# Kernel tuning notes

Hardware: AMD Instinct MI355X
Metric: run time of the kernel (lower is better)

## Reference

```python
import jax, jax.numpy as jnp
import numpy as np

L, H, C, V, T_BLK = 12, 12, 768, 50257, 1024
D = C // H  # head dim = 64


def _layernorm(x, g, b, eps=1e-5):
    m = jnp.mean(x, axis=-1, keepdims=True)
    v = jnp.mean(jnp.square(x - m), axis=-1, keepdims=True)
    return (x - m) * jax.lax.rsqrt(v + eps) * g + b


def setup_inputs() -> dict:
    key = jax.random.key(0)
    ks = jax.random.split(key, 8)
    B, T = 8, 1024
    s = 0.02
    sp = 0.02 / np.sqrt(2 * L)  # c_proj special init
    return {
        "idx": jax.random.randint(ks[0], (B, T), 0, V, dtype=jnp.int32),
        "wte": jax.random.normal(ks[1], (V, C), jnp.float32) * s,
        "wpe": jax.random.normal(ks[2], (T_BLK, C), jnp.float32) * s,
        "ln1_g": jnp.ones((L, C), jnp.float32),
        "ln1_b": jnp.zeros((L, C), jnp.float32),
        "w_qkv": jax.random.normal(ks[3], (L, C, 3 * C), jnp.float32) * s,
        "b_qkv": jnp.zeros((L, 3 * C), jnp.float32),
        "w_ao": jax.random.normal(ks[4], (L, C, C), jnp.float32) * sp,
        "b_ao": jnp.zeros((L, C), jnp.float32),
        "ln2_g": jnp.ones((L, C), jnp.float32),
        "ln2_b": jnp.zeros((L, C), jnp.float32),
        "w_fc": jax.random.normal(ks[5], (L, C, 4 * C), jnp.float32) * s,
        "b_fc": jnp.zeros((L, 4 * C), jnp.float32),
        "w_mo": jax.random.normal(ks[6], (L, 4 * C, C), jnp.float32) * sp,
        "b_mo": jnp.zeros((L, C), jnp.float32),
        "lnf_g": jnp.ones((C,), jnp.float32),
        "lnf_b": jnp.zeros((C,), jnp.float32),
    }


def reference(idx, wte, wpe, ln1_g, ln1_b, w_qkv, b_qkv, w_ao, b_ao,
              ln2_g, ln2_b, w_fc, b_fc, w_mo, b_mo, lnf_g, lnf_b):
    B, T = idx.shape
    scale = 1.0 / np.sqrt(D)
    causal = jnp.tril(jnp.ones((T, T), dtype=bool))  # [T,T]

    x = wte[idx] + wpe[:T]  # [B,T,C]

    def block(x, p):
        g1, b1, wq, bq, wo, bo, g2, b2_, wf, bf, w2, b2m = p
        h = _layernorm(x, g1, b1)
        qkv = h @ wq + bq  # [B,T,3C]
        q, k, v = jnp.split(qkv, 3, axis=-1)
        q = q.reshape(B, T, H, D)
        k = k.reshape(B, T, H, D)
        v = v.reshape(B, T, H, D)
        att = jnp.einsum('bqhd,bkhd->bhqk', q, k) * scale
        att = jnp.where(causal, att, -jnp.inf)
        att = jax.nn.softmax(att, axis=-1)
        y = jnp.einsum('bhqk,bkhd->bqhd', att, v).reshape(B, T, C)
        x = x + y @ wo + bo
        h2 = _layernorm(x, g2, b2_)
        x = x + jax.nn.gelu(h2 @ wf + bf, approximate=False) @ w2 + b2m
        return x, None

    params = (ln1_g, ln1_b, w_qkv, b_qkv, w_ao, b_ao,
              ln2_g, ln2_b, w_fc, b_fc, w_mo, b_mo)
    x, _ = jax.lax.scan(block, x, params)

    x = _layernorm(x, lnf_g, lnf_b)
    # inference path: logits only for last position, lm_head tied to wte
    logits = x[:, -1:, :] @ wte.T  # [B,1,V]
    return logits
```

## Files before the change

### kernel.cpp

```cpp
#include <hip/hip_runtime.h>

#define B_ 8
#define T_ 1024
#define C_ 768
#define H_ 12
#define L_ 12
#define V_ 50257

typedef __bf16 bf16_t;
typedef __bf16 bf16x8 __attribute__((ext_vector_type(8)));
typedef __bf16 bf16x4 __attribute__((ext_vector_type(4)));
typedef float f32x4 __attribute__((ext_vector_type(4)));

__device__ __forceinline__ unsigned short f2bf(float f) {
  bf16_t h = (bf16_t)f;
  return __builtin_bit_cast(unsigned short, h);
}

__device__ __forceinline__ unsigned short bfbits(bf16_t h) {
  return __builtin_bit_cast(unsigned short, h);
}

template<int CTRL>
__device__ __forceinline__ float dppf(float x) {
  return __builtin_bit_cast(float, __builtin_amdgcn_update_dpp(
      0, __builtin_bit_cast(int, x), CTRL, 0xF, 0xF, true));
}
__device__ __forceinline__ float red16_max(float x) {
  x = fmaxf(x, dppf<0xB1>(x));
  x = fmaxf(x, dppf<0x4E>(x));
  x = fmaxf(x, dppf<0x124>(x));
  x = fmaxf(x, dppf<0x128>(x));
  return x;
}
__device__ __forceinline__ float red16_sum(float x) {
  x += dppf<0xB1>(x);
  x += dppf<0x4E>(x);
  x += dppf<0x124>(x);
  x += dppf<0x128>(x);
  return x;
}

__global__ __launch_bounds__(192) void embed_kernel(
    const int* __restrict__ idx, const float* __restrict__ wte,
    const float* __restrict__ wpe, float* __restrict__ xf)
{
  const int bt = blockIdx.x;
  const int t = bt & (T_ - 1);
  const int tok = idx[bt];
  const int c4 = threadIdx.x << 2;
  float4 a = *(const float4*)(wte + (size_t)tok * C_ + c4);
  float4 p = *(const float4*)(wpe + (size_t)t * C_ + c4);
  float4 r; r.x = a.x + p.x; r.y = a.y + p.y; r.z = a.z + p.z; r.w = a.w + p.w;
  *(float4*)(xf + (size_t)bt * C_ + c4) = r;
}

template<bool LAST>
__global__ __launch_bounds__(256) void ln_kernel(
    const float* __restrict__ x, const float* __restrict__ gw,
    const float* __restrict__ bw, unsigned short* __restrict__ obf,
    float* __restrict__ of)
{
  __shared__ float red[8];
  const size_t row = LAST ? ((size_t)blockIdx.x * T_ + (T_ - 1)) : (size_t)blockIdx.x;
  const float* xr = x + row * C_;
  const int t = threadIdx.x;
  float v0 = xr[t], v1 = xr[t + 256], v2 = xr[t + 512];
  float s = v0 + v1 + v2;
  #pragma unroll
  for (int off = 32; off; off >>= 1) s += __shfl_xor(s, off);
  if ((t & 63) == 0) red[t >> 6] = s;
  __syncthreads();
  const float mean = (red[0] + red[1] + red[2] + red[3]) * (1.0f / C_);
  const float d0 = v0 - mean, d1 = v1 - mean, d2 = v2 - mean;
  float ss = d0 * d0 + d1 * d1 + d2 * d2;
  #pragma unroll
  for (int off = 32; off; off >>= 1) ss += __shfl_xor(ss, off);
  if ((t & 63) == 0) red[4 + (t >> 6)] = ss;
  __syncthreads();
  const float var = (red[4] + red[5] + red[6] + red[7]) * (1.0f / C_);
  const float rs = rsqrtf(var + 1e-5f);
  float o0 = d0 * rs * gw[t] + bw[t];
  float o1 = d1 * rs * gw[t + 256] + bw[t + 256];
  float o2 = d2 * rs * gw[t + 512] + bw[t + 512];
  if (LAST) {
    float* orow = of + (size_t)blockIdx.x * C_;
    orow[t] = o0; orow[t + 256] = o1; orow[t + 512] = o2;
  } else {
    unsigned short* orow = obf + row * C_;
    orow[t] = f2bf(o0); orow[t + 256] = f2bf(o1); orow[t + 512] = f2bf(o2);
  }
}

__global__ __launch_bounds__(256) void cvtw4_kernel(
    const float* __restrict__ wq, const float* __restrict__ wa,
    const float* __restrict__ wf, const float* __restrict__ wm,
    unsigned short* __restrict__ out)
{
  __shared__ float tile[32][33];
  const int i = blockIdx.x;
  const float* W; unsigned short* Wt; int K, N, tix;
  if (i < 1728)      { W = wq; Wt = out;                 K = C_;     N = 3 * C_; tix = i; }
  else if (i < 2304) { W = wa; Wt = out + 3 * C_ * C_;   K = C_;     N = C_;     tix = i - 1728; }
  else if (i < 4608) { W = wf; Wt = out + 4 * C_ * C_;   K = C_;     N = 4 * C_; tix = i - 2304; }
  else               { W = wm; Wt = out + 8 * C_ * C_;   K = 4 * C_; N = C_;     tix = i - 4608; }
  const int ntx = N >> 5;
  const int kb = (tix / ntx) << 5, nb = (tix % ntx) << 5;
  const int t = threadIdx.x;
  {
    const int k = t >> 3, n4 = (t & 7) << 2;
    float4 v = *(const float4*)(W + (size_t)(kb + k) * N + nb + n4);
    tile[k][n4] = v.x; tile[k][n4 + 1] = v.y; tile[k][n4 + 2] = v.z; tile[k][n4 + 3] = v.w;
  }
  __syncthreads();
  {
    const int n = t >> 3, k4 = (t & 7) << 2;
    ushort4 o;
    o.x = f2bf(tile[k4][n]);     o.y = f2bf(tile[k4 + 1][n]);
    o.z = f2bf(tile[k4 + 2][n]); o.w = f2bf(tile[k4 + 3][n]);
    *(ushort4*)(Wt + (size_t)(nb + n) * K + kb + k4) = o;
  }
}

template<int EPI>
__global__ __launch_bounds__(256) void gemm_bt(
    const unsigned short* __restrict__ A, const unsigned short* __restrict__ Bt,
    const float* __restrict__ bias, float* __restrict__ Cf,
    unsigned short* __restrict__ Cb, int M, int N, int K)
{
  __shared__ unsigned short As[128 * 32];
  __shared__ unsigned short Bs[128 * 32];
  const int tid = threadIdx.x;
  const int lane = tid & 63;
  const int w = tid >> 6;
  const int wr = w >> 1, wc = w & 1;
  const int m0 = blockIdx.y * 128;
  const int n0 = blockIdx.x * 128;
  const int l15 = lane & 15, l4 = lane >> 4;

  f32x4 acc[4][4] = {};

  const int srow = lane >> 2;
  const int schunk = lane & 3;
  const size_t aBase = (size_t)(m0 + w * 16 + srow) * K + schunk * 8;
  const size_t bBase = (size_t)(n0 + w * 16 + srow) * K + schunk * 8;
  unsigned short* sA = As + (w * 16) * 32;
  unsigned short* sB = Bs + (w * 16) * 32;

  const int nk = K >> 5;
  for (int kt = 0; kt < nk; ++kt) {
    const int k0 = kt << 5;
    __syncthreads();
    __builtin_amdgcn_global_load_lds(
        (const __attribute__((address_space(1))) unsigned int*)(A + aBase + k0),
        (__attribute__((address_space(3))) unsigned int*)(sA), 16, 0, 0);
    __builtin_amdgcn_global_load_lds(
        (const __attribute__((address_space(1))) unsigned int*)(A + aBase + (size_t)64 * K + k0),
        (__attribute__((address_space(3))) unsigned int*)(sA + 64 * 32), 16, 0, 0);
    __builtin_amdgcn_global_load_lds(
        (const __attribute__((address_space(1))) unsigned int*)(Bt + bBase + k0),
        (__attribute__((address_space(3))) unsigned int*)(sB), 16, 0, 0);
    __builtin_amdgcn_global_load_lds(
        (const __attribute__((address_space(1))) unsigned int*)(Bt + bBase + (size_t)64 * K + k0),
        (__attribute__((address_space(3))) unsigned int*)(sB + 64 * 32), 16, 0, 0);
    __syncthreads();

    bf16x8 af[4], bfr[4];
    const unsigned short* aw = As + wr * 64 * 32;
    const unsigned short* bw = Bs + wc * 64 * 32;
    #pragma unroll
    for (int mf = 0; mf < 4; ++mf)
      af[mf] = *(const bf16x8*)(aw + (mf * 16 + l15) * 32 + l4 * 8);
    #pragma unroll
    for (int nf = 0; nf < 4; ++nf)
      bfr[nf] = *(const bf16x8*)(bw + (nf * 16 + l15) * 32 + l4 * 8);
    #pragma unroll
    for (int mf = 0; mf < 4; ++mf) {
      #pragma unroll
      for (int nf = 0; nf < 4; ++nf)
        acc[mf][nf] = __builtin_amdgcn_mfma_f32_16x16x32_bf16(af[mf], bfr[nf], acc[mf][nf], 0, 0, 0);
    }
  }

  #pragma unroll
  for (int mf = 0; mf < 4; ++mf) {
    #pragma unroll
    for (int nf = 0; nf < 4; ++nf) {
      const int col = n0 + wc * 64 + nf * 16 + l15;
      const float bv = bias[col];
      int hh = 0, dd = 0;
      unsigned short* qkvo = nullptr;
      if constexpr (EPI == 3) {
        const int which = col / C_;
        const int rem = col - which * C_;
        hh = rem >> 6; dd = rem & 63;
        qkvo = Cb + (size_t)which * ((size_t)B_ * H_ * T_ * 64);
      }
      #pragma unroll
      for (int i = 0; i < 4; ++i) {
        const int row = m0 + wr * 64 + mf * 16 + l4 * 4 + i;
        float v = acc[mf][nf][i] + bv;
        if constexpr (EPI == 0) {
          Cf[(size_t)row * N + col] = v;
        } else if constexpr (EPI == 1) {
          Cf[(size_t)row * N + col] += v;
        } else if constexpr (EPI == 2) {
          float g = 0.5f * v * (1.0f + erff(v * 0.70710678118f));
          Cb[(size_t)row * N + col] = f2bf(g);
        } else {
          const int bb = row >> 10, tt = row & (T_ - 1);
          qkvo[(((size_t)bb * H_ + hh) * T_ + tt) * 64 + dd] = f2bf(v);
        }
      }
    }
  }
}

__global__ __launch_bounds__(256) void attn_kernel(
    const unsigned short* __restrict__ Qb, const unsigned short* __restrict__ Kb,
    const unsigned short* __restrict__ Vb, unsigned short* __restrict__ y)
{
  const int pb = blockIdx.x / 96;
  const int bh = blockIdx.x % 96;
  const int h = bh % H_;
  const int b = bh / H_;
  const int tid = threadIdx.x, lane = tid & 63, w = tid >> 6;
  const int l15 = lane & 15, l4 = lane >> 4;

  const int qw = (w < 2) ? (pb * 64 + w * 32) : ((15 - pb) * 64 + (w - 2) * 32);
  const int NT = (17 - pb) >> 1;

  __shared__ unsigned short Ks[128 * 64];
  __shared__ unsigned short Vt[64 * 136];
  __shared__ unsigned short Pb[4][32 * 74];

  const unsigned short* qp = Qb + ((size_t)bh * T_ + qw) * 64;
  bf16x8 qf[2][2];
  #pragma unroll
  for (int mf = 0; mf < 2; ++mf)
    #pragma unroll
    for (int ks = 0; ks < 2; ++ks)
      qf[mf][ks] = *(const bf16x8*)(qp + (mf * 16 + l15) * 64 + ks * 32 + l4 * 8);

  f32x4 o[2][4] = {};
  float mrow[2][4], lrow[2][4];
  #pragma unroll
  for (int mf = 0; mf < 2; ++mf)
    #pragma unroll
    for (int i = 0; i < 4; ++i) { mrow[mf][i] = -1e30f; lrow[mf][i] = 0.0f; }

  const unsigned short* kb0 = Kb + (size_t)bh * T_ * 64;
  const unsigned short* vb0 = Vb + (size_t)bh * T_ * 64;
  const int ck = w;
  const int skey = lane;
  const int sw = (skey & 7);

  bf16x8 kr0, kr1, kr2, kr3, vr0, vr1, vr2, vr3;
  {
    const unsigned short* kp = kb0 + (size_t)skey * 64;
    const unsigned short* vp = vb0 + (size_t)skey * 64;
    kr0 = *(const bf16x8*)(kp + ck * 8);
    kr1 = *(const bf16x8*)(kp + (ck + 4) * 8);
    kr2 = *(const bf16x8*)(kp + 64 * 64 + ck * 8);
    kr3 = *(const bf16x8*)(kp + 64 * 64 + (ck + 4) * 8);
    vr0 = *(const bf16x8*)(vp + ck * 8);
    vr1 = *(const bf16x8*)(vp + (ck + 4) * 8);
    vr2 = *(const bf16x8*)(vp + 64 * 64 + ck * 8);
    vr3 = *(const bf16x8*)(vp + 64 * 64 + (ck + 4) * 8);
  }

  for (int kt = 0; kt < NT; ++kt) {
    const int k0 = kt << 7;
    __syncthreads();
    *(bf16x8*)(Ks + skey * 64 + ((ck ^ sw) * 8)) = kr0;
    *(bf16x8*)(Ks + skey * 64 + (((ck + 4) ^ sw) * 8)) = kr1;
    *(bf16x8*)(Ks + (skey + 64) * 64 + ((ck ^ sw) * 8)) = kr2;
    *(bf16x8*)(Ks + (skey + 64) * 64 + (((ck + 4) ^ sw) * 8)) = kr3;
    #pragma unroll
    for (int j = 0; j < 8; ++j) {
      Vt[(ck * 8 + j) * 136 + skey]            = bfbits(vr0[j]);
      Vt[((ck + 4) * 8 + j) * 136 + skey]      = bfbits(vr1[j]);
      Vt[(ck * 8 + j) * 136 + skey + 64]       = bfbits(vr2[j]);
      Vt[((ck + 4) * 8 + j) * 136 + skey + 64] = bfbits(vr3[j]);
    }
    __syncthreads();
    if (kt + 1 < NT) {
      const int kn = (kt + 1) << 7;
      const unsigned short* kp = kb0 + (size_t)(kn + skey) * 64;
      const unsigned short* vp = vb0 + (size_t)(kn + skey) * 64;
      kr0 = *(const bf16x8*)(kp + ck * 8);
      kr1 = *(const bf16x8*)(kp + (ck + 4) * 8);
      kr2 = *(const bf16x8*)(kp + 64 * 64 + ck * 8);
      kr3 = *(const bf16x8*)(kp + 64 * 64 + (ck + 4) * 8);
      vr0 = *(const bf16x8*)(vp + ck * 8);
      vr1 = *(const bf16x8*)(vp + (ck + 4) * 8);
      vr2 = *(const bf16x8*)(vp + 64 * 64 + ck * 8);
      vr3 = *(const bf16x8*)(vp + 64 * 64 + (ck + 4) * 8);
    }

    #pragma unroll
    for (int h2 = 0; h2 < 2; ++h2) {
      const int kh0 = k0 + h2 * 64;
      if (kh0 > qw + 31) continue;

      f32x4 s[2][4] = {};
      __builtin_amdgcn_s_setprio(1);
      #pragma unroll
      for (int ks = 0; ks < 2; ++ks) {
        #pragma unroll
        for (int nfk = 0; nfk < 4; ++nfk) {
          const int key = h2 * 64 + nfk * 16 + l15;
          bf16x8 kf = *(const bf16x8*)(Ks + key * 64 + ((((ks << 2) | l4) ^ (l15 & 7)) * 8));
          #pragma unroll
          for (int mf = 0; mf < 2; ++mf)
            s[mf][nfk] = __builtin_amdgcn_mfma_f32_16x16x32_bf16(qf[mf][ks], kf, s[mf][nfk], 0, 0, 0);
        }
      }
      __builtin_amdgcn_s_setprio(0);

      #pragma unroll
      for (int mf = 0; mf < 2; ++mf) {
        const int qrow = qw + mf * 16 + l4 * 4;
        const bool fullt = (kh0 + 63) <= (qw + mf * 16);
        float alpha[4];
        float pvv[4][4];
        #pragma unroll
        for (int i = 0; i < 4; ++i) {
          const int q = qrow + i;
          float sv[4], tm = -1e30f;
          #pragma unroll
          for (int nfk = 0; nfk < 4; ++nfk) {
            float x = s[mf][nfk][i] * 0.125f;
            sv[nfk] = fullt ? x : ((kh0 + nfk * 16 + l15 <= q) ? x : -1e30f);
            tm = fmaxf(tm, sv[nfk]);
          }
          tm = red16_max(tm);
          const float mnew = fmaxf(mrow[mf][i], tm);
          alpha[i] = __expf(mrow[mf][i] - mnew);
          mrow[mf][i] = mnew;
          float rsum = 0.0f;
          #pragma unroll
          for (int nfk = 0; nfk < 4; ++nfk) {
            const float p = __expf(sv[nfk] - mnew);
            pvv[nfk][i] = p; rsum += p;
          }
          rsum = red16_sum(rsum);
          lrow[mf][i] = lrow[mf][i] * alpha[i] + rsum;
        }
        #pragma unroll
        for (int nf = 0; nf < 4; ++nf)
          #pragma unroll
          for (int i = 0; i < 4; ++i)
            o[mf][nf][i] *= alpha[i];
        #pragma unroll
        for (int nfk = 0; nfk < 4; ++nfk)
          #pragma unroll
          for (int i = 0; i < 4; ++i)
            Pb[w][(mf * 16 + l4 * 4 + i) * 74 + nfk * 16 + l15] = f2bf(pvv[nfk][i]);
      }

      bf16x8 pa[2][2];
      #pragma unroll
      for (int mf = 0; mf < 2; ++mf)
        #pragma unroll
        for (int k2 = 0; k2 < 2; ++k2)
          pa[mf][k2] = *(const bf16x8*)(Pb[w] + (mf * 16 + l15) * 74 + k2 * 32 + l4 * 8);
      __builtin_amdgcn_s_setprio(1);
      #pragma unroll
      for (int nf = 0; nf < 4; ++nf) {
        const int d = nf * 16 + l15;
        #pragma unroll
        for (int k2 = 0; k2 < 2; ++k2) {
          bf16x8 vf = *(const bf16x8*)(Vt + d * 136 + h2 * 64 + k2 * 32 + l4 * 8);
          #pragma unroll
          for (int mf = 0; mf < 2; ++mf)
            o[mf][nf] = __builtin_amdgcn_mfma_f32_16x16x32_bf16(pa[mf][k2], vf, o[mf][nf], 0, 0, 0);
        }
      }
      __builtin_amdgcn_s_setprio(0);
    }
  }

  #pragma unroll
  for (int mf = 0; mf < 2; ++mf) {
    #pragma unroll
    for (int i = 0; i < 4; ++i) {
      const float inv = 1.0f / lrow[mf][i];
      const int q = qw + mf * 16 + l4 * 4 + i;
      unsigned short* yr = y + (size_t)(b * T_ + q) * C_ + h * 64;
      #pragma unroll
      for (int nf = 0; nf < 4; ++nf)
        yr[nf * 16 + l15] = f2bf(o[mf][nf][i] * inv);
    }
  }
}

__global__ __launch_bounds__(256) void head_kernel(
    const float* __restrict__ lnf, const float* __restrict__ wte,
    float* __restrict__ out)
{
  __shared__ float xs[B_ * C_];
  for (int i = threadIdx.x; i < B_ * C_; i += 256) xs[i] = lnf[i];
  __syncthreads();
  const int w = threadIdx.x >> 6, lane = threadIdx.x & 63;
  const int v = blockIdx.x * 4 + w;
  if (v >= V_) return;
  const float* wv = wte + (size_t)v * C_ + lane * 12;
  float4 w0 = *(const float4*)(wv);
  float4 w1 = *(const float4*)(wv + 4);
  float4 w2 = *(const float4*)(wv + 8);
  float acc[B_];
  #pragma unroll
  for (int bb = 0; bb < B_; ++bb) {
    const float* xr = xs + bb * C_ + lane * 12;
    float4 x0 = *(const float4*)(xr);
    float4 x1 = *(const float4*)(xr + 4);
    float4 x2 = *(const float4*)(xr + 8);
    acc[bb] = w0.x * x0.x + w0.y * x0.y + w0.z * x0.z + w0.w * x0.w
            + w1.x * x1.x + w1.y * x1.y + w1.z * x1.z + w1.w * x1.w
            + w2.x * x2.x + w2.y * x2.y + w2.z * x2.z + w2.w * x2.w;
  }
  #pragma unroll
  for (int off = 32; off; off >>= 1) {
    #pragma unroll
    for (int bb = 0; bb < B_; ++bb)
      acc[bb] += __shfl_xor(acc[bb], off);
  }
  if (lane == 0) {
    #pragma unroll
    for (int bb = 0; bb < B_; ++bb)
      out[(size_t)bb * V_ + v] = acc[bb];
  }
}

extern "C" void kernel_launch(void* const* d_in, const int* in_sizes, int n_in,
                              void* d_out, int out_size, void* d_ws, size_t ws_size,
                              hipStream_t stream)
{
  (void)in_sizes; (void)n_in; (void)out_size; (void)ws_size;
  const int*   idx   = (const int*)d_in[0];
  const float* wte   = (const float*)d_in[1];
  const float* wpe   = (const float*)d_in[2];
  const float* ln1_g = (const float*)d_in[3];
  const float* ln1_b = (const float*)d_in[4];
  const float* w_qkv = (const float*)d_in[5];
  const float* b_qkv = (const float*)d_in[6];
  const float* w_ao  = (const float*)d_in[7];
  const float* b_ao  = (const float*)d_in[8];
  const float* ln2_g = (const float*)d_in[9];
  const float* ln2_b = (const float*)d_in[10];
  const float* w_fc  = (const float*)d_in[11];
  const float* b_fc  = (const float*)d_in[12];
  const float* w_mo  = (const float*)d_in[13];
  const float* b_mo  = (const float*)d_in[14];
  const float* lnf_g = (const float*)d_in[15];
  const float* lnf_b = (const float*)d_in[16];

  char* ws = (char*)d_ws;
  size_t off = 0;
  auto wsalloc = [&](size_t bytes) -> void* {
    void* p = ws + off;
    off += (bytes + 255) & ~(size_t)255;
    return p;
  };
  const size_t SZH = (size_t)B_ * H_ * T_ * 64;
  float* xf             = (float*)wsalloc((size_t)B_ * T_ * C_ * 4);
  unsigned short* qkv3  = (unsigned short*)wsalloc(3 * SZH * 2);
  unsigned short* a_in  = (unsigned short*)wsalloc((size_t)B_ * T_ * C_ * 2);
  unsigned short* act2  = (unsigned short*)wsalloc((size_t)B_ * T_ * 4 * C_ * 2);
  unsigned short* wbuf  = (unsigned short*)wsalloc((size_t)12 * C_ * C_ * 2);
  float* lnfb           = (float*)wsalloc((size_t)B_ * C_ * 4);

  const size_t OFF_AO = (size_t)3 * C_ * C_;
  const size_t OFF_FC = (size_t)4 * C_ * C_;
  const size_t OFF_MO = (size_t)8 * C_ * C_;

  embed_kernel<<<B_ * T_, 192, 0, stream>>>(idx, wte, wpe, xf);

  for (int l = 0; l < L_; ++l) {
    ln_kernel<false><<<B_ * T_, 256, 0, stream>>>(xf, ln1_g + l * C_, ln1_b + l * C_, a_in, nullptr);
    cvtw4_kernel<<<6912, 256, 0, stream>>>(
        w_qkv + (size_t)l * C_ * 3 * C_, w_ao + (size_t)l * C_ * C_,
        w_fc + (size_t)l * C_ * 4 * C_, w_mo + (size_t)l * 4 * C_ * C_, wbuf);
    gemm_bt<3><<<dim3(3 * C_ / 128, B_ * T_ / 128), 256, 0, stream>>>(a_in, wbuf, b_qkv + l * 3 * C_, nullptr, qkv3, B_ * T_, 3 * C_, C_);
    attn_kernel<<<8 * B_ * H_, 256, 0, stream>>>(qkv3, qkv3 + SZH, qkv3 + 2 * SZH, a_in);
    gemm_bt<1><<<dim3(C_ / 128, B_ * T_ / 128), 256, 0, stream>>>(a_in, wbuf + OFF_AO, b_ao + l * C_, xf, nullptr, B_ * T_, C_, C_);
    ln_kernel<false><<<B_ * T_, 256, 0, stream>>>(xf, ln2_g + l * C_, ln2_b + l * C_, a_in, nullptr);
    gemm_bt<2><<<dim3(4 * C_ / 128, B_ * T_ / 128), 256, 0, stream>>>(a_in, wbuf + OFF_FC, b_fc + l * 4 * C_, nullptr, act2, B_ * T_, 4 * C_, C_);
    gemm_bt<1><<<dim3(C_ / 128, B_ * T_ / 128), 256, 0, stream>>>(act2, wbuf + OFF_MO, b_mo + l * C_, xf, nullptr, B_ * T_, C_, 4 * C_);
  }

  ln_kernel<true><<<B_, 256, 0, stream>>>(xf, lnf_g, lnf_b, nullptr, lnfb);
  head_kernel<<<(V_ + 3) / 4, 256, 0, stream>>>(lnfb, wte, (float*)d_out);
}
```

Measured before the change: 4.259 ms.

## Double-buffer GEMM LDS tiles with BK=64, XOR swizzle, and XCD-aware block remap

Rewrites the bf16 MFMA GEMM main loop to use double-buffered LDS tiles with K-step 64. The next tile is prefetched via global_load_lds while the current one is computed, with a partial vmcnt wait replacing the full sync pair. Adds an XOR swizzle on the LDS chunk index to cut bank conflicts, s_setprio around the MFMA bursts, and a 1D grid remapped so consecutive blocks land on the same XCD. LDS use grows to 64KB per block with launch_bounds(256,2), which may limit occupancy.

```diff
diff --git a/kernel.cpp b/kernel.cpp
--- a/kernel.cpp
+++ b/kernel.cpp
@@ -123,64 +123,84 @@
 }
 
 template<int EPI>
-__global__ __launch_bounds__(256) void gemm_bt(
+__global__ __launch_bounds__(256, 2) void gemm_bt(
     const unsigned short* __restrict__ A, const unsigned short* __restrict__ Bt,
     const float* __restrict__ bias, float* __restrict__ Cf,
-    unsigned short* __restrict__ Cb, int M, int N, int K)
-{
-  __shared__ unsigned short As[128 * 32];
-  __shared__ unsigned short Bs[128 * 32];
+    unsigned short* __restrict__ Cb, int M, int N, int K, int nx)
+{
+  __shared__ unsigned short As[2][128 * 64];
+  __shared__ unsigned short Bs[2][128 * 64];
   const int tid = threadIdx.x;
   const int lane = tid & 63;
   const int w = tid >> 6;
   const int wr = w >> 1, wc = w & 1;
-  const int m0 = blockIdx.y * 128;
-  const int n0 = blockIdx.x * 128;
   const int l15 = lane & 15, l4 = lane >> 4;
+  const int swz = lane & 7;
+
+  const int nwg = gridDim.x;
+  int wg = blockIdx.x;
+  wg = (wg & 7) * (nwg >> 3) + (wg >> 3);
+  const int mblk = wg / nx;
+  const int nblk = wg - mblk * nx;
+  const int m0 = mblk * 128, n0 = nblk * 128;
 
   f32x4 acc[4][4] = {};
 
-  const int srow = lane >> 2;
-  const int schunk = lane & 3;
-  const size_t aBase = (size_t)(m0 + w * 16 + srow) * K + schunk * 8;
-  const size_t bBase = (size_t)(n0 + w * 16 + srow) * K + schunk * 8;
-  unsigned short* sA = As + (w * 16) * 32;
-  unsigned short* sB = Bs + (w * 16) * 32;
-
-  const int nk = K >> 5;
-  for (int kt = 0; kt < nk; ++kt) {
-    const int k0 = kt << 5;
-    __syncthreads();
-    __builtin_amdgcn_global_load_lds(
-        (const __attribute__((address_space(1))) unsigned int*)(A + aBase + k0),
-        (__attribute__((address_space(3))) unsigned int*)(sA), 16, 0, 0);
-    __builtin_amdgcn_global_load_lds(
-        (const __attribute__((address_space(1))) unsigned int*)(A + aBase + (size_t)64 * K + k0),
-        (__attribute__((address_space(3))) unsigned int*)(sA + 64 * 32), 16, 0, 0);
-    __builtin_amdgcn_global_load_lds(
-        (const __attribute__((address_space(1))) unsigned int*)(Bt + bBase + k0),
-        (__attribute__((address_space(3))) unsigned int*)(sB), 16, 0, 0);
-    __builtin_amdgcn_global_load_lds(
-        (const __attribute__((address_space(1))) unsigned int*)(Bt + bBase + (size_t)64 * K + k0),
-        (__attribute__((address_space(3))) unsigned int*)(sB + 64 * 32), 16, 0, 0);
-    __syncthreads();
-
-    bf16x8 af[4], bfr[4];
-    const unsigned short* aw = As + wr * 64 * 32;
-    const unsigned short* bw = Bs + wc * 64 * 32;
-    #pragma unroll
-    for (int mf = 0; mf < 4; ++mf)
-      af[mf] = *(const bf16x8*)(aw + (mf * 16 + l15) * 32 + l4 * 8);
-    #pragma unroll
-    for (int nf = 0; nf < 4; ++nf)
-      bfr[nf] = *(const bf16x8*)(bw + (nf * 16 + l15) * 32 + l4 * 8);
-    #pragma unroll
-    for (int mf = 0; mf < 4; ++mf) {
+  const int srow = lane >> 3;
+  const int schunk = (lane & 7) ^ srow;
+  const unsigned short* aSrc = A + (size_t)(m0 + w * 32 + srow) * K + schunk * 8;
+  const unsigned short* bSrc = Bt + (size_t)(n0 + w * 32 + srow) * K + schunk * 8;
+  const int ldsRowBase = (w * 32) * 64;
+
+  auto stage = [&](int kt, int p) {
+    const int k0 = kt << 6;
+    #pragma unroll
+    for (int j = 0; j < 4; ++j)
+      __builtin_amdgcn_global_load_lds(
+          (const __attribute__((address_space(1))) unsigned int*)(aSrc + (size_t)j * 8 * K + k0),
+          (__attribute__((address_space(3))) unsigned int*)(&As[p][ldsRowBase + j * 8 * 64]), 16, 0, 0);
+    #pragma unroll
+    for (int j = 0; j < 4; ++j)
+      __builtin_amdgcn_global_load_lds(
+          (const __attribute__((address_space(1))) unsigned int*)(bSrc + (size_t)j * 8 * K + k0),
+          (__attribute__((address_space(3))) unsigned int*)(&Bs[p][ldsRowBase + j * 8 * 64]), 16, 0, 0);
+  };
+
+  auto compute = [&](int p) {
+    const unsigned short* aw = &As[p][(wr * 64) * 64];
+    const unsigned short* bw2 = &Bs[p][(wc * 64) * 64];
+    #pragma unroll
+    for (int ks = 0; ks < 2; ++ks) {
+      bf16x8 af[4], bf[4];
+      #pragma unroll
+      for (int mf = 0; mf < 4; ++mf)
+        af[mf] = *(const bf16x8*)(aw + (mf * 16 + l15) * 64 + (((ks << 2) | l4) ^ swz) * 8);
       #pragma unroll
       for (int nf = 0; nf < 4; ++nf)
-        acc[mf][nf] = __builtin_amdgcn_mfma_f32_16x16x32_bf16(af[mf], bfr[nf], acc[mf][nf], 0, 0, 0);
+        bf[nf] = *(const bf16x8*)(bw2 + (nf * 16 + l15) * 64 + (((ks << 2) | l4) ^ swz) * 8);
+      __builtin_amdgcn_s_setprio(1);
+      #pragma unroll
+      for (int mf = 0; mf < 4; ++mf)
+        #pragma unroll
+        for (int nf = 0; nf < 4; ++nf)
+          acc[mf][nf] = __builtin_amdgcn_mfma_f32_16x16x32_bf16(af[mf], bf[nf], acc[mf][nf], 0, 0, 0);
+      __builtin_amdgcn_s_setprio(0);
     }
-  }
+  };
+
+  const int nk = K >> 6;
+  stage(0, 0);
+  for (int kt = 0; kt < nk - 1; ++kt) {
+    const int p = kt & 1;
+    stage(kt + 1, p ^ 1);
+    asm volatile("s_waitcnt vmcnt(8)" ::: "memory");
+    __builtin_amdgcn_s_barrier();
+    compute(p);
+    __builtin_amdgcn_s_barrier();
+  }
+  asm volatile("s_waitcnt vmcnt(0)" ::: "memory");
+  __builtin_amdgcn_s_barrier();
+  compute((nk - 1) & 1);
 
   #pragma unroll
   for (int mf = 0; mf < 4; ++mf) {
@@ -474,6 +494,7 @@
   const size_t OFF_AO = (size_t)3 * C_ * C_;
   const size_t OFF_FC = (size_t)4 * C_ * C_;
   const size_t OFF_MO = (size_t)8 * C_ * C_;
+  const int MROWS = B_ * T_;
 
   embed_kernel<<<B_ * T_, 192, 0, stream>>>(idx, wte, wpe, xf);
 
@@ -482,12 +503,12 @@
     cvtw4_kernel<<<6912, 256, 0, stream>>>(
         w_qkv + (size_t)l * C_ * 3 * C_, w_ao + (size_t)l * C_ * C_,
         w_fc + (size_t)l * C_ * 4 * C_, w_mo + (size_t)l * 4 * C_ * C_, wbuf);
-    gemm_bt<3><<<dim3(3 * C_ / 128, B_ * T_ / 128), 256, 0, stream>>>(a_in, wbuf, b_qkv + l * 3 * C_, nullptr, qkv3, B_ * T_, 3 * C_, C_);
+    gemm_bt<3><<<18 * 64, 256, 0, stream>>>(a_in, wbuf, b_qkv + l * 3 * C_, nullptr, qkv3, MROWS, 3 * C_, C_, 18);
     attn_kernel<<<8 * B_ * H_, 256, 0, stream>>>(qkv3, qkv3 + SZH, qkv3 + 2 * SZH, a_in);
-    gemm_bt<1><<<dim3(C_ / 128, B_ * T_ / 128), 256, 0, stream>>>(a_in, wbuf + OFF_AO, b_ao + l * C_, xf, nullptr, B_ * T_, C_, C_);
+    gemm_bt<1><<<6 * 64, 256, 0, stream>>>(a_in, wbuf + OFF_AO, b_ao + l * C_, xf, nullptr, MROWS, C_, C_, 6);
     ln_kernel<false><<<B_ * T_, 256, 0, stream>>>(xf, ln2_g + l * C_, ln2_b + l * C_, a_in, nullptr);
-    gemm_bt<2><<<dim3(4 * C_ / 128, B_ * T_ / 128), 256, 0, stream>>>(a_in, wbuf + OFF_FC, b_fc + l * 4 * C_, nullptr, act2, B_ * T_, 4 * C_, C_);
-    gemm_bt<1><<<dim3(C_ / 128, B_ * T_ / 128), 256, 0, stream>>>(act2, wbuf + OFF_MO, b_mo + l * C_, xf, nullptr, B_ * T_, C_, 4 * C_);
+    gemm_bt<2><<<24 * 64, 256, 0, stream>>>(a_in, wbuf + OFF_FC, b_fc + l * 4 * C_, nullptr, act2, MROWS, 4 * C_, C_, 24);
+    gemm_bt<1><<<6 * 64, 256, 0, stream>>>(act2, wbuf + OFF_MO, b_mo + l * C_, xf, nullptr, MROWS, C_, 4 * C_, 6);
   }
 
   ln_kernel<true><<<B_, 256, 0, stream>>>(xf, lnf_g, lnf_b, nullptr, lnfb);
```

Result: faster. 3.742 ms (-12.1%).
